# Kernel optimization log

Measured on AMD Instinct MI355X. Metric: run time of the kernel, lower is better.

## Reference

```python
import jax, jax.numpy as jnp
import numpy as np

B, C, Hf, Wf = 32, 512, 16, 16
S = Hf * Wf            # 256 kv tokens
D = 2048               # d_model
DIN = 512              # d_input (attention embed dim)
HEADS = 8
DH = DIN // HEADS
T = 50                 # iterations (internal ticks)
M = 25                 # memory_length
HH = 16                # memory_hidden_dims
NSA = 512              # n_synch_action
NSO = 512              # n_synch_out
OUT = 1000             # out_dims


def _ln(x, g, b, eps=1e-5):
    mu = x.mean(-1, keepdims=True)
    var = ((x - mu) ** 2).mean(-1, keepdims=True)
    return (x - mu) / jnp.sqrt(var + eps) * g + b


def _glu(x):
    a, b = jnp.split(x, 2, axis=-1)
    return a * jax.nn.sigmoid(b)


def setup_inputs() -> dict:
    key = jax.random.key(0)
    ki = iter(jax.random.split(key, 40))
    def rn(shape, s=0.02):
        return jax.random.normal(next(ki), shape, jnp.float32) * s
    inp = {}
    inp['x'] = jax.random.normal(next(ki), (B, C, Hf, Wf), jnp.float32)
    # kv_proj: Linear(C->DIN) + LayerNorm
    inp['kv_w'] = rn((C, DIN)); inp['kv_b'] = jnp.zeros((DIN,), jnp.float32)
    inp['ln_kv_g'] = jnp.ones((DIN,), jnp.float32); inp['ln_kv_b'] = jnp.zeros((DIN,), jnp.float32)
    # q_proj: Linear(NSA->DIN)
    inp['q_w'] = rn((NSA, DIN)); inp['q_b'] = jnp.zeros((DIN,), jnp.float32)
    # MultiheadAttention projections
    inp['Wq'] = rn((DIN, DIN)); inp['bq'] = jnp.zeros((DIN,), jnp.float32)
    inp['Wk'] = rn((DIN, DIN)); inp['bk'] = jnp.zeros((DIN,), jnp.float32)
    inp['Wv'] = rn((DIN, DIN)); inp['bv'] = jnp.zeros((DIN,), jnp.float32)
    inp['Wo'] = rn((DIN, DIN)); inp['bo'] = jnp.zeros((DIN,), jnp.float32)
    # synapse: Linear(DIN+D -> 2D) + GLU + LayerNorm(D)
    inp['syn_w'] = rn((DIN + D, 2 * D)); inp['syn_b'] = jnp.zeros((2 * D,), jnp.float32)
    inp['ln_syn_g'] = jnp.ones((D,), jnp.float32); inp['ln_syn_b'] = jnp.zeros((D,), jnp.float32)
    # per-neuron NLMs (SuperLinear weights: (in,out,N))
    inp['nlm_w1'] = rn((M, 2 * HH, D), 0.1); inp['nlm_b1'] = jnp.zeros((1, D, 2 * HH), jnp.float32)
    inp['nlm_w2'] = rn((HH, 2, D), 0.1); inp['nlm_b2'] = jnp.zeros((1, D, 2), jnp.float32)
    # output projector
    inp['out_w'] = rn((NSO, OUT)); inp['out_b'] = jnp.zeros((OUT,), jnp.float32)
    # learnable decay params (clamped to [0,15] in forward)
    inp['decay_action'] = jax.random.uniform(next(ki), (NSA,), jnp.float32)
    inp['decay_out'] = jax.random.uniform(next(ki), (NSO,), jnp.float32)
    # learned start state
    inp['start_trace'] = rn((D, M), 0.05)
    inp['start_act'] = rn((D,), 0.05)
    # random-pairing neuron indices (fixed at init in the original)
    inp['idx_la'] = jax.random.randint(next(ki), (NSA,), 0, D)
    inp['idx_ra'] = jax.random.randint(next(ki), (NSA,), 0, D)
    inp['idx_lo'] = jax.random.randint(next(ki), (NSO,), 0, D)
    inp['idx_ro'] = jax.random.randint(next(ki), (NSO,), 0, D)
    return inp


def reference(x, kv_w, kv_b, ln_kv_g, ln_kv_b, q_w, q_b, Wq, bq, Wk, bk, Wv, bv, Wo, bo,
              syn_w, syn_b, ln_syn_g, ln_syn_b, nlm_w1, nlm_b1, nlm_w2, nlm_b2,
              out_w, out_b, decay_action, decay_out, start_trace, start_act,
              idx_la, idx_ra, idx_lo, idx_ro):
    # featurise: identity backbone, flatten spatial to tokens, project to DIN
    feats = x.reshape(B, C, S).transpose(0, 2, 1)                 # (B,S,C)
    kv = _ln(feats @ kv_w + kv_b, ln_kv_g, ln_kv_b)               # (B,S,DIN)
    kh = (kv @ Wk + bk).reshape(B, S, HEADS, DH).transpose(0, 2, 1, 3)  # (B,H,S,DH)
    vh = (kv @ Wv + bv).reshape(B, S, HEADS, DH).transpose(0, 2, 1, 3)
    r_a = jnp.exp(-jnp.clip(decay_action, 0.0, 15.0))[None]       # (1,NSA)
    r_o = jnp.exp(-jnp.clip(decay_out, 0.0, 15.0))[None]          # (1,NSO)

    def nlm(trace):  # per-neuron MLP over the memory axis: (B,D,M) -> (B,D)
        h = _glu(jnp.einsum('bdm,mhd->bdh', trace, nlm_w1) + nlm_b1)
        return _glu(jnp.einsum('bdh,hod->bdo', h, nlm_w2) + nlm_b2)[..., 0]

    act0 = jnp.broadcast_to(start_act[None], (B, D))
    trace0 = jnp.broadcast_to(start_trace[None], (B, D, M))
    # out-synchronisation initialised from the start state (before the loop)
    a_o0 = act0[:, idx_lo] * act0[:, idx_ro]
    b_o0 = jnp.ones_like(a_o0)
    a_a0 = jnp.zeros((B, NSA), jnp.float32)
    b_a0 = jnp.zeros((B, NSA), jnp.float32)
    log_out = jnp.log(jnp.float32(OUT))
    scale = 1.0 / jnp.sqrt(jnp.float32(DH))

    def step(carry, _):
        trace, act, a_a, b_a, a_o, b_o = carry
        # action synchronisation (decayed pairwise products, sync = alpha/sqrt(beta))
        a_a = r_a * a_a + act[:, idx_la] * act[:, idx_ra]
        b_a = r_a * b_a + 1.0
        sync_a = a_a / jnp.sqrt(b_a)
        # attention readout (single query token)
        q = sync_a @ q_w + q_b                                    # (B,DIN)
        qh = (q @ Wq + bq).reshape(B, HEADS, 1, DH)
        attn = jax.nn.softmax(jnp.einsum('bhqd,bhkd->bhqk', qh, kh) * scale, -1)
        o = jnp.einsum('bhqk,bhkd->bhqd', attn, vh).transpose(0, 2, 1, 3).reshape(B, DIN)
        attn_out = o @ Wo + bo
        # synapse MLP -> new pre-activation state
        pre = jnp.concatenate([attn_out, act], axis=-1)           # (B,DIN+D)
        state = _ln(_glu(pre @ syn_w + syn_b), ln_syn_g, ln_syn_b)
        trace = jnp.concatenate([trace[:, :, 1:], state[:, :, None]], axis=-1)
        act = nlm(trace)                                          # (B,D)
        # output synchronisation + prediction
        a_o = r_o * a_o + act[:, idx_lo] * act[:, idx_ro]
        b_o = r_o * b_o + 1.0
        sync_o = a_o / jnp.sqrt(b_o)
        pred = sync_o @ out_w + out_b                             # (B,OUT)
        logp = jax.nn.log_softmax(pred, -1)
        ne = -(jnp.exp(logp) * logp).sum(-1) / log_out
        cert = jnp.stack([ne, 1.0 - ne], axis=-1)                 # (B,2)
        return (trace, act, a_a, b_a, a_o, b_o), (pred, cert, sync_o)

    _, (preds, certs, syncs) = jax.lax.scan(step, (trace0, act0, a_a0, b_a0, a_o0, b_o0), None, length=T)
    predictions = jnp.transpose(preds, (1, 2, 0))                 # (B,OUT,T)
    certainties = jnp.transpose(certs, (1, 2, 0))                 # (B,2,T)
    return predictions, certainties, syncs[-1]
```

## Files before the change

kernel.cpp:

```cpp
#include <hip/hip_runtime.h>
#include <math.h>

#define BB 32
#define CC 512
#define SS 256
#define DD 2048
#define DIN 512
#define NH 8
#define DHD 64
#define TT 50
#define MM 25
#define HHID 16
#define NSA 512
#define NSO 512
#define NOUT 1000

__device__ __forceinline__ unsigned short f2bf(float f) {
    unsigned u = __float_as_uint(f);
    u += 0x7fffu + ((u >> 16) & 1u);
    return (unsigned short)(u >> 16);
}
__device__ __forceinline__ float bf2f(unsigned short s) {
    return __uint_as_float((unsigned)s << 16);
}
__device__ __forceinline__ float blo(unsigned u) {
    return __uint_as_float(u << 16);
}
__device__ __forceinline__ float bhi(unsigned u) {
    return __uint_as_float(u & 0xffff0000u);
}

__global__ void init_kernel(const float* __restrict__ dec_a, const float* __restrict__ dec_o,
                            const float* __restrict__ start_act, const float* __restrict__ start_trace,
                            const int* __restrict__ idx_lo, const int* __restrict__ idx_ro,
                            float* __restrict__ r_a, float* __restrict__ r_o,
                            float* __restrict__ a_a, float* __restrict__ b_a,
                            float* __restrict__ a_o, float* __restrict__ b_o,
                            float* __restrict__ trace)
{
    int i = blockIdx.x * 256 + threadIdx.x;
    if (i < 512) {
        r_a[i] = expf(-fminf(fmaxf(dec_a[i], 0.f), 15.f));
        r_o[i] = expf(-fminf(fmaxf(dec_o[i], 0.f), 15.f));
    }
    if (i < BB * NSA) {
        a_a[i] = 0.f; b_a[i] = 0.f;
        int j = i & 511;
        a_o[i] = start_act[idx_lo[j]] * start_act[idx_ro[j]];
        b_o[i] = 1.f;
    }
    if (i < BB * MM * DD) {
        int rem = i % (MM * DD);
        int m = rem / DD, d = rem % DD;
        trace[i] = start_trace[d * MM + m];
    }
}

template<int AMODE, int SMODE>
__global__ void gemm64(const float* __restrict__ A, const float* __restrict__ Bm,
                       const float* __restrict__ bias, float* __restrict__ Cm,
                       int Mdim, int Ndim, int Kdim)
{
    __shared__ float As[16 * 65];
    __shared__ float Bs[16 * 64];
    int row0 = blockIdx.x * 64;
    int col0 = blockIdx.y * 64;
    int t = threadIdx.x;
    int tx = t & 15, ty = t >> 4;
    float acc[4][4] = {};
    for (int k0 = 0; k0 < Kdim; k0 += 16) {
        if (AMODE == 0) {
            for (int i = t; i < 1024; i += 256) {
                int kk = i & 15, r = i >> 4;
                As[kk * 65 + r] = A[(size_t)(row0 + r) * Kdim + k0 + kk];
            }
        } else {
            int b = row0 / SS, s0 = row0 % SS;
            for (int i = t; i < 1024; i += 256) {
                int r = i & 63, kk = i >> 6;
                As[kk * 65 + r] = A[((size_t)b * CC + k0 + kk) * SS + s0 + r];
            }
        }
        for (int i = t; i < 1024; i += 256) {
            int c = i & 63, kk = i >> 6;
            Bs[kk * 64 + c] = Bm[(size_t)(k0 + kk) * Ndim + col0 + c];
        }
        __syncthreads();
        #pragma unroll
        for (int kk = 0; kk < 16; ++kk) {
            float a[4], bb[4];
            #pragma unroll
            for (int i = 0; i < 4; i++) a[i] = As[kk * 65 + ty * 4 + i];
            #pragma unroll
            for (int j = 0; j < 4; j++) bb[j] = Bs[kk * 64 + tx * 4 + j];
            #pragma unroll
            for (int i = 0; i < 4; i++)
                #pragma unroll
                for (int j = 0; j < 4; j++) acc[i][j] += a[i] * bb[j];
        }
        __syncthreads();
    }
    #pragma unroll
    for (int i = 0; i < 4; i++)
        #pragma unroll
        for (int j = 0; j < 4; j++) {
            int row = row0 + ty * 4 + i, col = col0 + tx * 4 + j;
            float v = acc[i][j] + (bias ? bias[col] : 0.f);
            if (SMODE == 0) {
                Cm[(size_t)row * Ndim + col] = v;
            } else if (SMODE == 1) {
                int b = row / SS, s = row % SS, h = col >> 6, dh = col & 63;
                Cm[(((size_t)b * NH + h) * DHD + dh) * SS + s] = v;
            } else {
                int b = row / SS, s = row % SS, h = col >> 6, dh = col & 63;
                Cm[(((size_t)b * NH + h) * SS + s) * DHD + dh] = v;
            }
        }
}

__global__ void ln_rows(float* __restrict__ buf, const float* __restrict__ g,
                        const float* __restrict__ bta)
{
    int row = blockIdx.x, t = threadIdx.x;
    __shared__ float red[256];
    float v0 = buf[(size_t)row * 512 + t];
    float v1 = buf[(size_t)row * 512 + 256 + t];
    red[t] = v0 + v1; __syncthreads();
    for (int off = 128; off; off >>= 1) { if (t < off) red[t] += red[t + off]; __syncthreads(); }
    float mu = red[0] * (1.f / 512.f); __syncthreads();
    float d0 = v0 - mu, d1 = v1 - mu;
    red[t] = d0 * d0 + d1 * d1; __syncthreads();
    for (int off = 128; off; off >>= 1) { if (t < off) red[t] += red[t + off]; __syncthreads(); }
    float rstd = 1.f / sqrtf(red[0] * (1.f / 512.f) + 1e-5f);
    buf[(size_t)row * 512 + t]       = d0 * rstd * g[t] + bta[t];
    buf[(size_t)row * 512 + 256 + t] = d1 * rstd * g[t + 256] + bta[t + 256];
}

__global__ void bqq_kernel(const float* __restrict__ q_b, const float* __restrict__ Wq,
                           const float* __restrict__ bq, float* __restrict__ bqq)
{
    int c = blockIdx.x * 256 + threadIdx.x;
    if (c >= 512) return;
    float acc = bq[c];
    for (int k = 0; k < 512; k++) acc += q_b[k] * Wq[k * 512 + c];
    bqq[c] = acc;
}

__global__ void bias2_kernel(const float* __restrict__ bo, const float* __restrict__ syn_w,
                             const float* __restrict__ syn_b, float* __restrict__ bias2)
{
    int c = blockIdx.x * 256 + threadIdx.x;
    if (c >= 4096) return;
    float acc = syn_b[c];
    for (int k = 0; k < 512; k++) acc += bo[k] * syn_w[(size_t)k * 4096 + c];
    bias2[c] = acc;
}

__global__ void wt_build(const float* __restrict__ W2, const float* __restrict__ syn_w,
                         unsigned short* __restrict__ WTh)
{
    __shared__ float tile[32][33];
    int k0 = blockIdx.x * 32, c0 = blockIdx.y * 32;
    int t = threadIdx.x;
    int col = t & 31, rq = t >> 5;
    #pragma unroll
    for (int q = 0; q < 4; ++q) {
        int kk = q * 8 + rq;
        int k = k0 + kk;
        const float* src = (k < 512 ? W2 : syn_w) + (size_t)k * 4096 + c0;
        tile[kk][col] = src[col];
    }
    __syncthreads();
    #pragma unroll
    for (int q = 0; q < 4; ++q) {
        int cc = q * 8 + rq;
        WTh[(size_t)(c0 + cc) * 2560 + k0 + col] = f2bf(tile[col][cc]);
    }
}

__global__ void conv_kernel(const float* __restrict__ khT, const float* __restrict__ vh,
                            const float* __restrict__ w1,
                            unsigned short* __restrict__ khTh, unsigned short* __restrict__ vhh,
                            unsigned short* __restrict__ w1h)
{
    int i = blockIdx.x * 256 + threadIdx.x;
    khTh[i] = f2bf(khT[i]);
    vhh[i]  = f2bf(vh[i]);
    if (i < 25 * 32 * DD) w1h[i] = f2bf(w1[i]);
}

__global__ void act0_kernel(const float* __restrict__ start_act, float* __restrict__ act0slot)
{
    int i = blockIdx.x * 256 + threadIdx.x;
    if (i < BB * DD) act0slot[i] = start_act[i & (DD - 1)];
}

__global__ void pad_outw(const float* __restrict__ out_w, const float* __restrict__ out_b,
                         float* __restrict__ out_wp, float* __restrict__ out_bp)
{
    int i = blockIdx.x * 256 + threadIdx.x;
    if (i < 512 * 1024) {
        int r = i >> 10, c = i & 1023;
        out_wp[i] = (c < 1000) ? out_w[r * 1000 + c] : 0.f;
    }
    if (i < 1024) out_bp[i] = (i < 1000) ? out_b[i] : 0.f;
}

__global__ __launch_bounds__(256) void k1_front(
    const float* __restrict__ act, const int* __restrict__ la, const int* __restrict__ ra,
    const float* __restrict__ r_a,
    const float* __restrict__ aold, const float* __restrict__ bold,
    float* __restrict__ anew, float* __restrict__ bnew,
    const float* __restrict__ Wqq, const float* __restrict__ bqq,
    const unsigned short* __restrict__ khTh, const unsigned short* __restrict__ vhh,
    float* __restrict__ obuf)
{
    __shared__ float sa[512];
    __shared__ float qp[256];
    __shared__ float qs[64];
    __shared__ float ps[256];
    __shared__ float red[256];
    int bh = blockIdx.x, b = bh >> 3, h = bh & 7;
    int tid = threadIdx.x;
    const float* actb = act + b * DD;
    for (int j = tid; j < 512; j += 256) {
        float p = actb[la[j]] * actb[ra[j]];
        float r = r_a[j];
        float aa = r * aold[b * 512 + j] + p;
        float bb = r * bold[b * 512 + j] + 1.f;
        sa[j] = aa / sqrtf(bb);
        if (h == 0) { anew[b * 512 + j] = aa; bnew[b * 512 + j] = bb; }
    }
    __syncthreads();
    {
        int cl = tid & 63, q = tid >> 6;
        const float* wcol = Wqq + h * 64 + cl;
        float acc = 0.f;
        #pragma unroll 8
        for (int k = q * 128; k < q * 128 + 128; ++k)
            acc += sa[k] * wcol[k * 512];
        qp[tid] = acc;
    }
    __syncthreads();
    if (tid < 64)
        qs[tid] = qp[tid] + qp[tid + 64] + qp[tid + 128] + qp[tid + 192] + bqq[h * 64 + tid];
    __syncthreads();
    const unsigned short* kb = khTh + (size_t)bh * 64 * 256;
    float sc = 0.f;
    #pragma unroll 8
    for (int dh = 0; dh < 64; ++dh) sc += qs[dh] * bf2f(kb[dh * 256 + tid]);
    sc *= 0.125f;
    red[tid] = sc; __syncthreads();
    for (int off = 128; off; off >>= 1) { if (tid < off) red[tid] = fmaxf(red[tid], red[tid + off]); __syncthreads(); }
    float mx = red[0]; __syncthreads();
    float e = expf(sc - mx);
    red[tid] = e; __syncthreads();
    for (int off = 128; off; off >>= 1) { if (tid < off) red[tid] += red[tid + off]; __syncthreads(); }
    float inv = 1.f / red[0];
    ps[tid] = e * inv;
    __syncthreads();
    int dh = tid & 63, ch = tid >> 6;
    const unsigned short* vb = vhh + (size_t)bh * 256 * 64;
    float acc = 0.f;
    for (int s = ch * 64; s < ch * 64 + 64; ++s) acc += ps[s] * bf2f(vb[s * 64 + dh]);
    red[tid] = acc; __syncthreads();
    if (tid < 128) red[tid] += red[tid + 128];
    __syncthreads();
    if (tid < 64) obuf[b * 512 + h * 64 + tid] = red[tid] + red[tid + 64];
}

__global__ __launch_bounds__(256) void k2_glu(
    const float* __restrict__ obuf, const float* __restrict__ act,
    const unsigned short* __restrict__ WTh, const float* __restrict__ bias2,
    float* __restrict__ glbufT, float* __restrict__ partials)
{
    __shared__ float As[2 * 32 * 160];
    int tid = threadIdx.x, blk = blockIdx.x;
    int kh = tid >> 7;
    int cpair = (tid >> 5) & 3;
    int r = tid & 31;
    int c = blk * 4 + cpair;
    const unsigned short* wta = WTh + (size_t)c * 2560 + kh * 1280;
    const unsigned short* wtb = WTh + (size_t)(c + 2048) * 2560 + kh * 1280;
    float acc_a = 0.f, acc_b = 0.f;
    for (int ri = 0; ri < 8; ++ri) {
        __syncthreads();
        #pragma unroll
        for (int q = 0; q < 10; ++q) {
            int i = tid + q * 256;
            int hh = i / 1280;
            int rem = i - hh * 1280;
            int rr = rem / 40, kg = rem - (rem / 40) * 40;
            int k = hh * 1280 + ri * 160 + kg * 4;
            float4 v;
            if (k < 512) v = *(const float4*)(obuf + rr * 512 + k);
            else         v = *(const float4*)(act + rr * 2048 + (k - 512));
            *(float4*)(As + hh * 5120 + rr * 160 + ((kg ^ (rr & 7)) << 2)) = v;
        }
        __syncthreads();
        const float* Ar = As + kh * 5120 + r * 160;
        const unsigned short* wtaa = wta + ri * 160;
        const unsigned short* wtbb = wtb + ri * 160;
        int sw = r & 7;
        #pragma unroll 4
        for (int kc = 0; kc < 20; ++kc) {
            uint4 wa = *(const uint4*)(wtaa + kc * 8);
            uint4 wb = *(const uint4*)(wtbb + kc * 8);
            float4 a0 = *(const float4*)(Ar + (((2 * kc) ^ sw) << 2));
            float4 a1 = *(const float4*)(Ar + (((2 * kc + 1) ^ sw) << 2));
            acc_a += a0.x * blo(wa.x) + a0.y * bhi(wa.x) + a0.z * blo(wa.y) + a0.w * bhi(wa.y)
                   + a1.x * blo(wa.z) + a1.y * bhi(wa.z) + a1.z * blo(wa.w) + a1.w * bhi(wa.w);
            acc_b += a0.x * blo(wb.x) + a0.y * bhi(wb.x) + a0.z * blo(wb.y) + a0.w * bhi(wb.y)
                   + a1.x * blo(wb.z) + a1.y * bhi(wb.z) + a1.z * blo(wb.w) + a1.w * bhi(wb.w);
        }
    }
    __syncthreads();
    float* red_a = As;
    float* red_b = As + 128;
    float* gls   = As + 256;
    float* gl2s  = As + 384;
    if (kh == 1) {
        red_a[cpair * 32 + r] = acc_a;
        red_b[cpair * 32 + r] = acc_b;
    }
    __syncthreads();
    if (kh == 0) {
        float ua = acc_a + red_a[cpair * 32 + r] + bias2[c];
        float ub = acc_b + red_b[cpair * 32 + r] + bias2[c + 2048];
        float gl = ua * (1.f / (1.f + expf(-ub)));
        glbufT[c * 32 + r] = gl;
        gls[cpair * 32 + r] = gl;
        gl2s[cpair * 32 + r] = gl * gl;
    }
    __syncthreads();
    if (tid < 32) {
        float s = 0.f, s2 = 0.f;
        #pragma unroll
        for (int cp = 0; cp < 4; ++cp) { s += gls[cp * 32 + tid]; s2 += gl2s[cp * 32 + tid]; }
        partials[blk * 64 + tid * 2]     = s;
        partials[blk * 64 + tid * 2 + 1] = s2;
    }
}

#define K4_LDS_FLOATS (12800 + 2176 + 256 + 256 + 16)
__global__ __launch_bounds__(256) void k4_nlm(
    const float* __restrict__ glbufT, const float* __restrict__ partials,
    const float* __restrict__ g, const float* __restrict__ bta,
    float* __restrict__ trace,
    const unsigned short* __restrict__ w1h, const float* __restrict__ b1,
    const float* __restrict__ w2, const float* __restrict__ b2,
    float* __restrict__ actout, int t_iter)
{
    extern __shared__ float lds[];
    float* wlds  = lds;
    float* cross = lds + 12800;
    float* r1 = lds + 14976;
    float* r2 = lds + 15232;
    float* sm = lds + 15488;
    int tid = threadIdx.x, blk = blockIdx.x;
    int dtile = blk & 127, bgrp = blk >> 7;
    int d0 = dtile * 16, b0 = bgrp * 8;
    int hh = tid >> 7;
    int b_l = (tid >> 4) & 7;
    int d_l = tid & 15;
    int b = b0 + b_l, d = d0 + d_l;

    for (int q = 0; q < 50; ++q) {
        int i = tid + q * 256;
        wlds[i] = bf2f(w1h[(size_t)(i >> 4) * 2048 + d0 + (i & 15)]);
    }
    {
        int bb = tid >> 5, j = tid & 31;
        int bstat = b0 + bb;
        float s = 0.f, s2 = 0.f;
        #pragma unroll
        for (int q = 0; q < 16; ++q) {
            int kblk = j + 32 * q;
            s  += partials[kblk * 64 + bstat * 2];
            s2 += partials[kblk * 64 + bstat * 2 + 1];
        }
        r1[tid] = s; r2[tid] = s2;
        __syncthreads();
        for (int off = 16; off; off >>= 1) {
            if (j < off) { r1[tid] += r1[tid + off]; r2[tid] += r2[tid + off]; }
            __syncthreads();
        }
        if (j == 0) {
            float mu = r1[tid] * (1.f / 2048.f);
            float var = r2[tid] * (1.f / 2048.f) - mu * mu;
            sm[bb * 2] = mu;
            sm[bb * 2 + 1] = 1.f / sqrtf(var + 1e-5f);
        }
        __syncthreads();
    }
    float mu = sm[b_l * 2], rstd = sm[b_l * 2 + 1];
    float gl = glbufT[d * 32 + b];
    float nv = (gl - mu) * rstd * g[d] + bta[d];
    int newrow = t_iter % MM;
    if (hh == 0) trace[((size_t)b * MM + newrow) * DD + d] = nv;

    float hp[16];
    {
        const float* b1d = b1 + d * 32 + hh * 16;
        #pragma unroll
        for (int h = 0; h < 16; h++) hp[h] = b1d[h];
    }
    const float* trb = trace + (size_t)b * MM * DD + d;
    for (int m = 0; m < 24; m++) {
        int mph = (t_iter + 1 + m) % 25;
        float tv = trb[(size_t)mph * DD];
        const float* wm = wlds + (m * 32 + hh * 16) * 16 + d_l;
        #pragma unroll
        for (int h = 0; h < 16; h++) hp[h] += tv * wm[h * 16];
    }
    {
        const float* wm = wlds + (24 * 32 + hh * 16) * 16 + d_l;
        #pragma unroll
        for (int h = 0; h < 16; h++) hp[h] += nv * wm[h * 16];
    }
    if (hh == 1) {
        float* cx = cross + (b_l * 16 + d_l) * 17;
        #pragma unroll
        for (int h = 0; h < 16; h++) cx[h] = hp[h];
    }
    __syncthreads();
    if (hh == 0) {
        const float* cx = cross + (b_l * 16 + d_l) * 17;
        float o0 = b2[d * 2], o1 = b2[d * 2 + 1];
        #pragma unroll
        for (int h = 0; h < 16; h++) {
            float hv = hp[h] * (1.f / (1.f + expf(-cx[h])));
            o0 += hv * w2[((size_t)h * 2) * DD + d];
            o1 += hv * w2[((size_t)h * 2 + 1) * DD + d];
        }
        actout[b * DD + d] = o0 * (1.f / (1.f + expf(-o1)));
    }
}

__global__ __launch_bounds__(256) void k_syncscan(
    const float* __restrict__ acthist, const int* __restrict__ lo, const int* __restrict__ ro,
    const float* __restrict__ r_o,
    const float* __restrict__ a_o0, const float* __restrict__ b_o0,
    float* __restrict__ so_hist, float* __restrict__ out_sync)
{
    int idx = blockIdx.x * 256 + threadIdx.x;
    int b = idx >> 9, j = idx & 511;
    float aa = a_o0[idx], bb = b_o0[idx];
    float rr = r_o[j];
    int il = lo[j], ir = ro[j];
    const float* ah = acthist + (size_t)(BB * DD) + b * DD;
    float s = 0.f;
    for (int t = 0; t < TT; ++t) {
        float p = ah[il] * ah[ir];
        aa = rr * aa + p;
        bb = rr * bb + 1.f;
        s = aa / sqrtf(bb);
        so_hist[(size_t)t * (BB * 512) + idx] = s;
        ah += BB * DD;
    }
    out_sync[idx] = s;
}

__global__ __launch_bounds__(256) void k6_cert(
    const float* __restrict__ predt, float* __restrict__ d_out)
{
    int t_iter = blockIdx.x >> 5, b = blockIdx.x & 31, t = threadIdx.x;
    __shared__ float red[256];
    const float* pr = predt + ((size_t)t_iter * 32 + b) * 1024;
    float pv[4];
    float mx = -1e30f;
    #pragma unroll
    for (int ii = 0; ii < 4; ++ii) {
        int c = t + ii * 256;
        float v = -1e30f;
        if (c < 1000) {
            v = pr[c];
            d_out[(size_t)b * NOUT * TT + (size_t)c * TT + t_iter] = v;
        }
        pv[ii] = v;
        mx = fmaxf(mx, v);
    }
    red[t] = mx; __syncthreads();
    for (int off = 128; off; off >>= 1) { if (t < off) red[t] = fmaxf(red[t], red[t + off]); __syncthreads(); }
    mx = red[0]; __syncthreads();
    float s1 = 0.f, s2 = 0.f;
    #pragma unroll
    for (int ii = 0; ii < 4; ++ii) {
        int c = t + ii * 256;
        if (c < 1000) { float xx = pv[ii] - mx; float e = expf(xx); s1 += e; s2 += e * xx; }
    }
    red[t] = s1; __syncthreads();
    for (int off = 128; off; off >>= 1) { if (t < off) red[t] += red[t + off]; __syncthreads(); }
    s1 = red[0]; __syncthreads();
    red[t] = s2; __syncthreads();
    for (int off = 128; off; off >>= 1) { if (t < off) red[t] += red[t + off]; __syncthreads(); }
    s2 = red[0];
    if (t == 0) {
        float ne = -(s2 / s1 - logf(s1)) * (1.f / logf(1000.f));
        size_t base = (size_t)BB * NOUT * TT + (size_t)b * 2 * TT + t_iter;
        d_out[base] = ne;
        d_out[base + TT] = 1.f - ne;
    }
}

extern "C" void kernel_launch(void* const* d_in, const int* in_sizes, int n_in,
                              void* d_out, int out_size, void* d_ws, size_t ws_size,
                              hipStream_t stream)
{
    const float* x        = (const float*)d_in[0];
    const float* kv_w     = (const float*)d_in[1];
    const float* kv_b     = (const float*)d_in[2];
    const float* ln_kv_g  = (const float*)d_in[3];
    const float* ln_kv_b  = (const float*)d_in[4];
    const float* q_w      = (const float*)d_in[5];
    const float* q_b      = (const float*)d_in[6];
    const float* Wq       = (const float*)d_in[7];
    const float* bq       = (const float*)d_in[8];
    const float* Wk       = (const float*)d_in[9];
    const float* bk       = (const float*)d_in[10];
    const float* Wv       = (const float*)d_in[11];
    const float* bv       = (const float*)d_in[12];
    const float* Wo       = (const float*)d_in[13];
    const float* bo       = (const float*)d_in[14];
    const float* syn_w    = (const float*)d_in[15];
    const float* syn_b    = (const float*)d_in[16];
    const float* ln_syn_g = (const float*)d_in[17];
    const float* ln_syn_b = (const float*)d_in[18];
    const float* nlm_w1   = (const float*)d_in[19];
    const float* nlm_b1   = (const float*)d_in[20];
    const float* nlm_w2   = (const float*)d_in[21];
    const float* nlm_b2   = (const float*)d_in[22];
    const float* out_w    = (const float*)d_in[23];
    const float* out_b    = (const float*)d_in[24];
    const float* dec_a    = (const float*)d_in[25];
    const float* dec_o    = (const float*)d_in[26];
    const float* start_tr = (const float*)d_in[27];
    const float* start_ac = (const float*)d_in[28];
    const int*   idx_la   = (const int*)d_in[29];
    const int*   idx_ra   = (const int*)d_in[30];
    const int*   idx_lo   = (const int*)d_in[31];
    const int*   idx_ro   = (const int*)d_in[32];
    float* out = (float*)d_out;

    float* w = (float*)d_ws;
    float* kvbuf = w;            w += (size_t)8192 * 512;
    float* khT   = w;            w += (size_t)8192 * 512;
    float* vhb   = w;            w += (size_t)8192 * 512;
    float* Wqq   = w;            w += (size_t)512 * 512;
    float* bqq   = w;            w += 512;
    float* W2    = w;            w += (size_t)512 * 4096;
    float* bias2 = w;            w += 4096;
    float* r_a   = w;            w += 512;
    float* r_o   = w;            w += 512;
    float* a_a   = w;            w += 2 * BB * NSA;
    float* b_a   = w;            w += 2 * BB * NSA;
    float* a_o   = w;            w += BB * NSO;
    float* b_o   = w;            w += BB * NSO;
    float* trace = w;            w += (size_t)BB * MM * DD;
    float* obuf  = w;            w += BB * DIN;
    float* glbufT = w;           w += (size_t)DD * BB;
    float* partials = w;         w += 512 * 32 * 2;
    unsigned short* WTh  = (unsigned short*)w;  w += (size_t)4096 * 2560 / 2;
    unsigned short* khTh = (unsigned short*)w;  w += (size_t)8192 * 512 / 2;
    unsigned short* vhh  = (unsigned short*)w;  w += (size_t)8192 * 512 / 2;
    unsigned short* w1h  = (unsigned short*)w;  w += (size_t)25 * 32 * DD / 2;

    float* acthist = kvbuf;
    float* so_hist = vhb;
    float* predt   = vhb + 819200;
    float* out_wp  = khT;
    float* out_bp  = khT + 524288;

    init_kernel<<<6400, 256, 0, stream>>>(dec_a, dec_o, start_ac, start_tr, idx_lo, idx_ro,
                                          r_a, r_o, a_a, b_a, a_o, b_o, trace);
    gemm64<1, 0><<<dim3(128, 8), 256, 0, stream>>>(x, kv_w, kv_b, kvbuf, 8192, 512, 512);
    ln_rows<<<8192, 256, 0, stream>>>(kvbuf, ln_kv_g, ln_kv_b);
    gemm64<0, 1><<<dim3(128, 8), 256, 0, stream>>>(kvbuf, Wk, bk, khT, 8192, 512, 512);
    gemm64<0, 2><<<dim3(128, 8), 256, 0, stream>>>(kvbuf, Wv, bv, vhb, 8192, 512, 512);
    gemm64<0, 0><<<dim3(8, 8), 256, 0, stream>>>(q_w, Wq, nullptr, Wqq, 512, 512, 512);
    bqq_kernel<<<2, 256, 0, stream>>>(q_b, Wq, bq, bqq);
    gemm64<0, 0><<<dim3(8, 64), 256, 0, stream>>>(Wo, syn_w, nullptr, W2, 512, 4096, 512);
    bias2_kernel<<<16, 256, 0, stream>>>(bo, syn_w, syn_b, bias2);
    wt_build<<<dim3(80, 128), 256, 0, stream>>>(W2, syn_w, WTh);
    conv_kernel<<<16384, 256, 0, stream>>>(khT, vhb, nlm_w1, khTh, vhh, w1h);
    act0_kernel<<<256, 256, 0, stream>>>(start_ac, acthist);

    float* out_sync = out + (size_t)BB * NOUT * TT + (size_t)BB * 2 * TT;

    static int lds_attr_set = 0;
    if (!lds_attr_set) {
        hipFuncSetAttribute(reinterpret_cast<const void*>(k4_nlm),
                            hipFuncAttributeMaxDynamicSharedMemorySize,
                            K4_LDS_FLOATS * 4);
        lds_attr_set = 1;
    }

    for (int t = 0; t < TT; ++t) {
        int par = t & 1;
        const float* act_t = acthist + (size_t)t * (BB * DD);
        float* act_n = acthist + (size_t)(t + 1) * (BB * DD);
        k1_front<<<256, 256, 0, stream>>>(act_t, idx_la, idx_ra, r_a,
                                          a_a + par * (BB * 512), b_a + par * (BB * 512),
                                          a_a + (par ^ 1) * (BB * 512), b_a + (par ^ 1) * (BB * 512),
                                          Wqq, bqq, khTh, vhh, obuf);
        k2_glu<<<512, 256, 0, stream>>>(obuf, act_t, WTh, bias2, glbufT, partials);
        k4_nlm<<<512, 256, K4_LDS_FLOATS * 4, stream>>>(glbufT, partials,
                                            ln_syn_g, ln_syn_b, trace,
                                            w1h, nlm_b1, nlm_w2, nlm_b2, act_n, t);
    }

    k_syncscan<<<64, 256, 0, stream>>>(acthist, idx_lo, idx_ro, r_o, a_o, b_o,
                                       so_hist, out_sync);
    pad_outw<<<2048, 256, 0, stream>>>(out_w, out_b, out_wp, out_bp);
    gemm64<0, 0><<<dim3(25, 16), 256, 0, stream>>>(so_hist, out_wp, out_bp, predt,
                                                   1600, 1024, 512);
    k6_cert<<<1600, 256, 0, stream>>>(predt, out);
}
```

Before: 4.405 ms.

## Fuse per-tick attention, GLU and NLM kernels with grid-wide atomic barriers

Merges the three per-iteration kernels into one persistent-style launch of 512 blocks. The phases are separated by a software grid barrier built on an atomic counter. Intermediate buffers are indexed per tick so there is no reuse hazard across launches. The K/V projection GEMMs now write bf16 directly, which removes the separate conversion pass. This cuts launch count and launch gaps per tick, but the code depends on all 512 blocks being co-resident, and the spin barriers and cross-block visibility through relaxed atomics may add latency or risk deadlock.

Measured after the change: 5.317 ms. +20.7%, slower.

```diff
diff --git a/kernel.cpp b/kernel.cpp
--- a/kernel.cpp
+++ b/kernel.cpp
@@ -15,6 +15,9 @@
 #define NSO 512
 #define NOUT 1000
 
+#define NBLKT 512
+#define KT_LDS_FLOATS 15504
+
 __device__ __forceinline__ unsigned short f2bf(float f) {
     unsigned u = __float_as_uint(f);
     u += 0x7fffu + ((u >> 16) & 1u);
@@ -30,15 +33,34 @@
     return __uint_as_float(u & 0xffff0000u);
 }
 
+__device__ __forceinline__ void cst(float* p, float v) {
+    __hip_atomic_store(p, v, __ATOMIC_RELAXED, __HIP_MEMORY_SCOPE_AGENT);
+}
+
+__device__ __forceinline__ void gsync(unsigned* __restrict__ ctr, unsigned target)
+{
+    __threadfence_block();
+    __syncthreads();
+    if (threadIdx.x == 0) {
+        __hip_atomic_fetch_add(ctr, 1u, __ATOMIC_RELAXED, __HIP_MEMORY_SCOPE_AGENT);
+        while (__hip_atomic_load(ctr, __ATOMIC_RELAXED, __HIP_MEMORY_SCOPE_AGENT) < target)
+            __builtin_amdgcn_s_sleep(4);
+        asm volatile("" ::: "memory");
+    }
+    __syncthreads();
+}
+
 __global__ void init_kernel(const float* __restrict__ dec_a, const float* __restrict__ dec_o,
                             const float* __restrict__ start_act, const float* __restrict__ start_trace,
                             const int* __restrict__ idx_lo, const int* __restrict__ idx_ro,
+                            unsigned* __restrict__ bar,
                             float* __restrict__ r_a, float* __restrict__ r_o,
                             float* __restrict__ a_a, float* __restrict__ b_a,
                             float* __restrict__ a_o, float* __restrict__ b_o,
                             float* __restrict__ trace)
 {
     int i = blockIdx.x * 256 + threadIdx.x;
+    if (i < 16) bar[i] = 0u;
     if (i < 512) {
         r_a[i] = expf(-fminf(fmaxf(dec_a[i], 0.f), 15.f));
         r_o[i] = expf(-fminf(fmaxf(dec_o[i], 0.f), 15.f));
@@ -108,12 +130,12 @@
             float v = acc[i][j] + (bias ? bias[col] : 0.f);
             if (SMODE == 0) {
                 Cm[(size_t)row * Ndim + col] = v;
-            } else if (SMODE == 1) {
+            } else if (SMODE == 3) {
                 int b = row / SS, s = row % SS, h = col >> 6, dh = col & 63;
-                Cm[(((size_t)b * NH + h) * DHD + dh) * SS + s] = v;
-            } else {
+                ((unsigned short*)Cm)[(((size_t)b * NH + h) * DHD + dh) * SS + s] = f2bf(v);
+            } else if (SMODE == 4) {
                 int b = row / SS, s = row % SS, h = col >> 6, dh = col & 63;
-                Cm[(((size_t)b * NH + h) * SS + s) * DHD + dh] = v;
+                ((unsigned short*)Cm)[(((size_t)b * NH + h) * SS + s) * DHD + dh] = f2bf(v);
             }
         }
 }
@@ -178,14 +200,9 @@
     }
 }
 
-__global__ void conv_kernel(const float* __restrict__ khT, const float* __restrict__ vh,
-                            const float* __restrict__ w1,
-                            unsigned short* __restrict__ khTh, unsigned short* __restrict__ vhh,
-                            unsigned short* __restrict__ w1h)
+__global__ void conv_w1(const float* __restrict__ w1, unsigned short* __restrict__ w1h)
 {
     int i = blockIdx.x * 256 + threadIdx.x;
-    khTh[i] = f2bf(khT[i]);
-    vhh[i]  = f2bf(vh[i]);
     if (i < 25 * 32 * DD) w1h[i] = f2bf(w1[i]);
 }
 
@@ -206,234 +223,234 @@
     if (i < 1024) out_bp[i] = (i < 1000) ? out_b[i] : 0.f;
 }
 
-__global__ __launch_bounds__(256) void k1_front(
-    const float* __restrict__ act, const int* __restrict__ la, const int* __restrict__ ra,
+__global__ __launch_bounds__(256) void k_tick(
+    const float* __restrict__ act_t, float* __restrict__ act_n,
+    const int* __restrict__ la, const int* __restrict__ ra,
     const float* __restrict__ r_a,
     const float* __restrict__ aold, const float* __restrict__ bold,
     float* __restrict__ anew, float* __restrict__ bnew,
     const float* __restrict__ Wqq, const float* __restrict__ bqq,
     const unsigned short* __restrict__ khTh, const unsigned short* __restrict__ vhh,
-    float* __restrict__ obuf)
-{
-    __shared__ float sa[512];
-    __shared__ float qp[256];
-    __shared__ float qs[64];
-    __shared__ float ps[256];
-    __shared__ float red[256];
-    int bh = blockIdx.x, b = bh >> 3, h = bh & 7;
-    int tid = threadIdx.x;
-    const float* actb = act + b * DD;
-    for (int j = tid; j < 512; j += 256) {
-        float p = actb[la[j]] * actb[ra[j]];
-        float r = r_a[j];
-        float aa = r * aold[b * 512 + j] + p;
-        float bb = r * bold[b * 512 + j] + 1.f;
-        sa[j] = aa / sqrtf(bb);
-        if (h == 0) { anew[b * 512 + j] = aa; bnew[b * 512 + j] = bb; }
-    }
-    __syncthreads();
-    {
-        int cl = tid & 63, q = tid >> 6;
-        const float* wcol = Wqq + h * 64 + cl;
-        float acc = 0.f;
-        #pragma unroll 8
-        for (int k = q * 128; k < q * 128 + 128; ++k)
-            acc += sa[k] * wcol[k * 512];
-        qp[tid] = acc;
-    }
-    __syncthreads();
-    if (tid < 64)
-        qs[tid] = qp[tid] + qp[tid + 64] + qp[tid + 128] + qp[tid + 192] + bqq[h * 64 + tid];
-    __syncthreads();
-    const unsigned short* kb = khTh + (size_t)bh * 64 * 256;
-    float sc = 0.f;
-    #pragma unroll 8
-    for (int dh = 0; dh < 64; ++dh) sc += qs[dh] * bf2f(kb[dh * 256 + tid]);
-    sc *= 0.125f;
-    red[tid] = sc; __syncthreads();
-    for (int off = 128; off; off >>= 1) { if (tid < off) red[tid] = fmaxf(red[tid], red[tid + off]); __syncthreads(); }
-    float mx = red[0]; __syncthreads();
-    float e = expf(sc - mx);
-    red[tid] = e; __syncthreads();
-    for (int off = 128; off; off >>= 1) { if (tid < off) red[tid] += red[tid + off]; __syncthreads(); }
-    float inv = 1.f / red[0];
-    ps[tid] = e * inv;
-    __syncthreads();
-    int dh = tid & 63, ch = tid >> 6;
-    const unsigned short* vb = vhh + (size_t)bh * 256 * 64;
-    float acc = 0.f;
-    for (int s = ch * 64; s < ch * 64 + 64; ++s) acc += ps[s] * bf2f(vb[s * 64 + dh]);
-    red[tid] = acc; __syncthreads();
-    if (tid < 128) red[tid] += red[tid + 128];
-    __syncthreads();
-    if (tid < 64) obuf[b * 512 + h * 64 + tid] = red[tid] + red[tid + 64];
-}
-
-__global__ __launch_bounds__(256) void k2_glu(
-    const float* __restrict__ obuf, const float* __restrict__ act,
     const unsigned short* __restrict__ WTh, const float* __restrict__ bias2,
-    float* __restrict__ glbufT, float* __restrict__ partials)
-{
-    __shared__ float As[2 * 32 * 160];
-    int tid = threadIdx.x, blk = blockIdx.x;
-    int kh = tid >> 7;
-    int cpair = (tid >> 5) & 3;
-    int r = tid & 31;
-    int c = blk * 4 + cpair;
-    const unsigned short* wta = WTh + (size_t)c * 2560 + kh * 1280;
-    const unsigned short* wtb = WTh + (size_t)(c + 2048) * 2560 + kh * 1280;
-    float acc_a = 0.f, acc_b = 0.f;
-    for (int ri = 0; ri < 8; ++ri) {
-        __syncthreads();
-        #pragma unroll
-        for (int q = 0; q < 10; ++q) {
-            int i = tid + q * 256;
-            int hh = i / 1280;
-            int rem = i - hh * 1280;
-            int rr = rem / 40, kg = rem - (rem / 40) * 40;
-            int k = hh * 1280 + ri * 160 + kg * 4;
-            float4 v;
-            if (k < 512) v = *(const float4*)(obuf + rr * 512 + k);
-            else         v = *(const float4*)(act + rr * 2048 + (k - 512));
-            *(float4*)(As + hh * 5120 + rr * 160 + ((kg ^ (rr & 7)) << 2)) = v;
-        }
-        __syncthreads();
-        const float* Ar = As + kh * 5120 + r * 160;
-        const unsigned short* wtaa = wta + ri * 160;
-        const unsigned short* wtbb = wtb + ri * 160;
-        int sw = r & 7;
-        #pragma unroll 4
-        for (int kc = 0; kc < 20; ++kc) {
-            uint4 wa = *(const uint4*)(wtaa + kc * 8);
-            uint4 wb = *(const uint4*)(wtbb + kc * 8);
-            float4 a0 = *(const float4*)(Ar + (((2 * kc) ^ sw) << 2));
-            float4 a1 = *(const float4*)(Ar + (((2 * kc + 1) ^ sw) << 2));
-            acc_a += a0.x * blo(wa.x) + a0.y * bhi(wa.x) + a0.z * blo(wa.y) + a0.w * bhi(wa.y)
-                   + a1.x * blo(wa.z) + a1.y * bhi(wa.z) + a1.z * blo(wa.w) + a1.w * bhi(wa.w);
-            acc_b += a0.x * blo(wb.x) + a0.y * bhi(wb.x) + a0.z * blo(wb.y) + a0.w * bhi(wb.y)
-                   + a1.x * blo(wb.z) + a1.y * bhi(wb.z) + a1.z * blo(wb.w) + a1.w * bhi(wb.w);
-        }
-    }
-    __syncthreads();
-    float* red_a = As;
-    float* red_b = As + 128;
-    float* gls   = As + 256;
-    float* gl2s  = As + 384;
-    if (kh == 1) {
-        red_a[cpair * 32 + r] = acc_a;
-        red_b[cpair * 32 + r] = acc_b;
-    }
-    __syncthreads();
-    if (kh == 0) {
-        float ua = acc_a + red_a[cpair * 32 + r] + bias2[c];
-        float ub = acc_b + red_b[cpair * 32 + r] + bias2[c + 2048];
-        float gl = ua * (1.f / (1.f + expf(-ub)));
-        glbufT[c * 32 + r] = gl;
-        gls[cpair * 32 + r] = gl;
-        gl2s[cpair * 32 + r] = gl * gl;
-    }
-    __syncthreads();
-    if (tid < 32) {
-        float s = 0.f, s2 = 0.f;
-        #pragma unroll
-        for (int cp = 0; cp < 4; ++cp) { s += gls[cp * 32 + tid]; s2 += gl2s[cp * 32 + tid]; }
-        partials[blk * 64 + tid * 2]     = s;
-        partials[blk * 64 + tid * 2 + 1] = s2;
-    }
-}
-
-#define K4_LDS_FLOATS (12800 + 2176 + 256 + 256 + 16)
-__global__ __launch_bounds__(256) void k4_nlm(
-    const float* __restrict__ glbufT, const float* __restrict__ partials,
     const float* __restrict__ g, const float* __restrict__ bta,
     float* __restrict__ trace,
     const unsigned short* __restrict__ w1h, const float* __restrict__ b1,
     const float* __restrict__ w2, const float* __restrict__ b2,
-    float* __restrict__ actout, int t_iter)
+    float* __restrict__ obuf_t, float* __restrict__ gl_t, float* __restrict__ part_t,
+    unsigned* __restrict__ bar, int t_iter)
 {
     extern __shared__ float lds[];
-    float* wlds  = lds;
-    float* cross = lds + 12800;
-    float* r1 = lds + 14976;
-    float* r2 = lds + 15232;
-    float* sm = lds + 15488;
-    int tid = threadIdx.x, blk = blockIdx.x;
-    int dtile = blk & 127, bgrp = blk >> 7;
-    int d0 = dtile * 16, b0 = bgrp * 8;
-    int hh = tid >> 7;
-    int b_l = (tid >> 4) & 7;
-    int d_l = tid & 15;
-    int b = b0 + b_l, d = d0 + d_l;
-
-    for (int q = 0; q < 50; ++q) {
-        int i = tid + q * 256;
-        wlds[i] = bf2f(w1h[(size_t)(i >> 4) * 2048 + d0 + (i & 15)]);
-    }
+    const int blk = blockIdx.x;
+    const int tid = threadIdx.x;
+    const unsigned base = (unsigned)t_iter * (2u * NBLKT);
+
+    if (blk < 256) {
+        float* sa  = lds;
+        float* qp  = lds + 512;
+        float* qs  = lds + 768;
+        float* ps  = lds + 832;
+        float* red = lds + 1088;
+        int b = blk >> 3, h = blk & 7;
+        const float* actb = act_t + b * DD;
+        for (int j = tid; j < 512; j += 256) {
+            float p = actb[la[j]] * actb[ra[j]];
+            float r = r_a[j];
+            float aa = r * aold[b * 512 + j] + p;
+            float bb = r * bold[b * 512 + j] + 1.f;
+            sa[j] = aa / sqrtf(bb);
+            if (h == 0) { anew[b * 512 + j] = aa; bnew[b * 512 + j] = bb; }
+        }
+        __syncthreads();
+        {
+            int cl = tid & 63, q = tid >> 6;
+            const float* wcol = Wqq + h * 64 + cl;
+            float acc = 0.f;
+            #pragma unroll 8
+            for (int k = q * 128; k < q * 128 + 128; ++k)
+                acc += sa[k] * wcol[k * 512];
+            qp[tid] = acc;
+        }
+        __syncthreads();
+        if (tid < 64)
+            qs[tid] = qp[tid] + qp[tid + 64] + qp[tid + 128] + qp[tid + 192] + bqq[h * 64 + tid];
+        __syncthreads();
+        const unsigned short* kb = khTh + (size_t)blk * 64 * 256;
+        float sc = 0.f;
+        #pragma unroll 8
+        for (int dh = 0; dh < 64; ++dh) sc += qs[dh] * bf2f(kb[dh * 256 + tid]);
+        sc *= 0.125f;
+        red[tid] = sc; __syncthreads();
+        for (int off = 128; off; off >>= 1) { if (tid < off) red[tid] = fmaxf(red[tid], red[tid + off]); __syncthreads(); }
+        float mx = red[0]; __syncthreads();
+        float e = expf(sc - mx);
+        red[tid] = e; __syncthreads();
+        for (int off = 128; off; off >>= 1) { if (tid < off) red[tid] += red[tid + off]; __syncthreads(); }
+        float inv = 1.f / red[0];
+        ps[tid] = e * inv;
+        __syncthreads();
+        int dh = tid & 63, ch = tid >> 6;
+        const unsigned short* vb = vhh + (size_t)blk * 256 * 64;
+        float acc = 0.f;
+        for (int s = ch * 64; s < ch * 64 + 64; ++s) acc += ps[s] * bf2f(vb[s * 64 + dh]);
+        red[tid] = acc; __syncthreads();
+        if (tid < 128) red[tid] += red[tid + 128];
+        __syncthreads();
+        if (tid < 64) cst(&obuf_t[b * 512 + h * 64 + tid], red[tid] + red[tid + 64]);
+    }
+    gsync(bar, base + NBLKT);
+
     {
-        int bb = tid >> 5, j = tid & 31;
-        int bstat = b0 + bb;
-        float s = 0.f, s2 = 0.f;
-        #pragma unroll
-        for (int q = 0; q < 16; ++q) {
-            int kblk = j + 32 * q;
-            s  += partials[kblk * 64 + bstat * 2];
-            s2 += partials[kblk * 64 + bstat * 2 + 1];
-        }
-        r1[tid] = s; r2[tid] = s2;
-        __syncthreads();
-        for (int off = 16; off; off >>= 1) {
-            if (j < off) { r1[tid] += r1[tid + off]; r2[tid] += r2[tid + off]; }
+        float* As = lds;
+        int kh = tid >> 7;
+        int cpair = (tid >> 5) & 3;
+        int r = tid & 31;
+        int c = blk * 4 + cpair;
+        const unsigned short* wta = WTh + (size_t)c * 2560 + kh * 1280;
+        const unsigned short* wtb = WTh + (size_t)(c + 2048) * 2560 + kh * 1280;
+        float acc_a = 0.f, acc_b = 0.f;
+        for (int ri = 0; ri < 8; ++ri) {
             __syncthreads();
-        }
-        if (j == 0) {
-            float mu = r1[tid] * (1.f / 2048.f);
-            float var = r2[tid] * (1.f / 2048.f) - mu * mu;
-            sm[bb * 2] = mu;
-            sm[bb * 2 + 1] = 1.f / sqrtf(var + 1e-5f);
-        }
-        __syncthreads();
-    }
-    float mu = sm[b_l * 2], rstd = sm[b_l * 2 + 1];
-    float gl = glbufT[d * 32 + b];
-    float nv = (gl - mu) * rstd * g[d] + bta[d];
-    int newrow = t_iter % MM;
-    if (hh == 0) trace[((size_t)b * MM + newrow) * DD + d] = nv;
-
-    float hp[16];
+            #pragma unroll
+            for (int q = 0; q < 10; ++q) {
+                int i = tid + q * 256;
+                int hh = i / 1280;
+                int rem = i - hh * 1280;
+                int rr = rem / 40, kg = rem - (rem / 40) * 40;
+                int k = hh * 1280 + ri * 160 + kg * 4;
+                float4 v;
+                if (k < 512) v = *(const float4*)(obuf_t + rr * 512 + k);
+                else         v = *(const float4*)(act_t + rr * 2048 + (k - 512));
+                *(float4*)(As + hh * 5120 + rr * 160 + ((kg ^ (rr & 7)) << 2)) = v;
+            }
+            __syncthreads();
+            const float* Ar = As + kh * 5120 + r * 160;
+            const unsigned short* wtaa = wta + ri * 160;
+            const unsigned short* wtbb = wtb + ri * 160;
+            int sw = r & 7;
+            #pragma unroll 4
+            for (int kc = 0; kc < 20; ++kc) {
+                uint4 wa = *(const uint4*)(wtaa + kc * 8);
+                uint4 wb = *(const uint4*)(wtbb + kc * 8);
+                float4 a0 = *(const float4*)(Ar + (((2 * kc) ^ sw) << 2));
+                float4 a1 = *(const float4*)(Ar + (((2 * kc + 1) ^ sw) << 2));
+                acc_a += a0.x * blo(wa.x) + a0.y * bhi(wa.x) + a0.z * blo(wa.y) + a0.w * bhi(wa.y)
+                       + a1.x * blo(wa.z) + a1.y * bhi(wa.z) + a1.z * blo(wa.w) + a1.w * bhi(wa.w);
+                acc_b += a0.x * blo(wb.x) + a0.y * bhi(wb.x) + a0.z * blo(wb.y) + a0.w * bhi(wb.y)
+                       + a1.x * blo(wb.z) + a1.y * bhi(wb.z) + a1.z * blo(wb.w) + a1.w * bhi(wb.w);
+            }
+        }
+        __syncthreads();
+        float* red_a = lds;
+        float* red_b = lds + 128;
+        float* gls   = lds + 256;
+        float* gl2s  = lds + 384;
+        if (kh == 1) {
+            red_a[cpair * 32 + r] = acc_a;
+            red_b[cpair * 32 + r] = acc_b;
+        }
+        __syncthreads();
+        if (kh == 0) {
+            float ua = acc_a + red_a[cpair * 32 + r] + bias2[c];
+            float ub = acc_b + red_b[cpair * 32 + r] + bias2[c + 2048];
+            float gl = ua * (1.f / (1.f + expf(-ub)));
+            cst(&gl_t[c * 32 + r], gl);
+            gls[cpair * 32 + r] = gl;
+            gl2s[cpair * 32 + r] = gl * gl;
+        }
+        __syncthreads();
+        if (tid < 32) {
+            float s = 0.f, s2 = 0.f;
+            #pragma unroll
+            for (int cp = 0; cp < 4; ++cp) { s += gls[cp * 32 + tid]; s2 += gl2s[cp * 32 + tid]; }
+            cst(&part_t[blk * 64 + tid * 2], s);
+            cst(&part_t[blk * 64 + tid * 2 + 1], s2);
+        }
+    }
+    gsync(bar, base + 2 * NBLKT);
+
     {
-        const float* b1d = b1 + d * 32 + hh * 16;
-        #pragma unroll
-        for (int h = 0; h < 16; h++) hp[h] = b1d[h];
-    }
-    const float* trb = trace + (size_t)b * MM * DD + d;
-    for (int m = 0; m < 24; m++) {
-        int mph = (t_iter + 1 + m) % 25;
-        float tv = trb[(size_t)mph * DD];
-        const float* wm = wlds + (m * 32 + hh * 16) * 16 + d_l;
-        #pragma unroll
-        for (int h = 0; h < 16; h++) hp[h] += tv * wm[h * 16];
-    }
-    {
-        const float* wm = wlds + (24 * 32 + hh * 16) * 16 + d_l;
-        #pragma unroll
-        for (int h = 0; h < 16; h++) hp[h] += nv * wm[h * 16];
-    }
-    if (hh == 1) {
-        float* cx = cross + (b_l * 16 + d_l) * 17;
-        #pragma unroll
-        for (int h = 0; h < 16; h++) cx[h] = hp[h];
-    }
-    __syncthreads();
-    if (hh == 0) {
-        const float* cx = cross + (b_l * 16 + d_l) * 17;
-        float o0 = b2[d * 2], o1 = b2[d * 2 + 1];
-        #pragma unroll
-        for (int h = 0; h < 16; h++) {
-            float hv = hp[h] * (1.f / (1.f + expf(-cx[h])));
-            o0 += hv * w2[((size_t)h * 2) * DD + d];
-            o1 += hv * w2[((size_t)h * 2 + 1) * DD + d];
-        }
-        actout[b * DD + d] = o0 * (1.f / (1.f + expf(-o1)));
+        float* wlds  = lds;
+        float* cross = lds + 12800;
+        float* r1 = lds + 14976;
+        float* r2 = lds + 15232;
+        float* sm = lds + 15488;
+        int dtile = blk & 127, bgrp = blk >> 7;
+        int d0 = dtile * 16, b0 = bgrp * 8;
+        int hh = tid >> 7;
+        int b_l = (tid >> 4) & 7;
+        int d_l = tid & 15;
+        int b = b0 + b_l, d = d0 + d_l;
+
+        for (int q = 0; q < 50; ++q) {
+            int i = tid + q * 256;
+            wlds[i] = bf2f(w1h[(size_t)(i >> 4) * 2048 + d0 + (i & 15)]);
+        }
+        {
+            int bb = tid >> 5, j = tid & 31;
+            int bstat = b0 + bb;
+            float s = 0.f, s2 = 0.f;
+            #pragma unroll
+            for (int q = 0; q < 16; ++q) {
+                int kblk = j + 32 * q;
+                s  += part_t[kblk * 64 + bstat * 2];
+                s2 += part_t[kblk * 64 + bstat * 2 + 1];
+            }
+            r1[tid] = s; r2[tid] = s2;
+            __syncthreads();
+            for (int off = 16; off; off >>= 1) {
+                if (j < off) { r1[tid] += r1[tid + off]; r2[tid] += r2[tid + off]; }
+                __syncthreads();
+            }
+            if (j == 0) {
+                float mu = r1[tid] * (1.f / 2048.f);
+                float var = r2[tid] * (1.f / 2048.f) - mu * mu;
+                sm[bb * 2] = mu;
+                sm[bb * 2 + 1] = 1.f / sqrtf(var + 1e-5f);
+            }
+            __syncthreads();
+        }
+        float mu = sm[b_l * 2], rstd = sm[b_l * 2 + 1];
+        float gl = gl_t[d * 32 + b];
+        float nv = (gl - mu) * rstd * g[d] + bta[d];
+        int newrow = t_iter % MM;
+        if (hh == 0) trace[((size_t)b * MM + newrow) * DD + d] = nv;
+
+        float hp[16];
+        {
+            const float* b1d = b1 + d * 32 + hh * 16;
+            #pragma unroll
+            for (int h = 0; h < 16; h++) hp[h] = b1d[h];
+        }
+        const float* trb = trace + (size_t)b * MM * DD + d;
+        for (int m = 0; m < 24; m++) {
+            int mph = (t_iter + 1 + m) % 25;
+            float tv = trb[(size_t)mph * DD];
+            const float* wm = wlds + (m * 32 + hh * 16) * 16 + d_l;
+            #pragma unroll
+            for (int h = 0; h < 16; h++) hp[h] += tv * wm[h * 16];
+        }
+        {
+            const float* wm = wlds + (24 * 32 + hh * 16) * 16 + d_l;
+            #pragma unroll
+            for (int h = 0; h < 16; h++) hp[h] += nv * wm[h * 16];
+        }
+        if (hh == 1) {
+            float* cx = cross + (b_l * 16 + d_l) * 17;
+            #pragma unroll
+            for (int h = 0; h < 16; h++) cx[h] = hp[h];
+        }
+        __syncthreads();
+        if (hh == 0) {
+            const float* cx = cross + (b_l * 16 + d_l) * 17;
+            float o0 = b2[d * 2], o1 = b2[d * 2 + 1];
+            #pragma unroll
+            for (int h = 0; h < 16; h++) {
+                float hv = hp[h] * (1.f / (1.f + expf(-cx[h])));
+                o0 += hv * w2[((size_t)h * 2) * DD + d];
+                o1 += hv * w2[((size_t)h * 2 + 1) * DD + d];
+            }
+            act_n[b * DD + d] = o0 * (1.f / (1.f + expf(-o1)));
+        }
     }
 }
 
@@ -542,10 +559,11 @@
     const int*   idx_ro   = (const int*)d_in[32];
     float* out = (float*)d_out;
 
-    float* w = (float*)d_ws;
+    unsigned* bar = (unsigned*)d_ws;
+    float* w = (float*)d_ws + 64;
     float* kvbuf = w;            w += (size_t)8192 * 512;
-    float* khT   = w;            w += (size_t)8192 * 512;
-    float* vhb   = w;            w += (size_t)8192 * 512;
+    float* bigA  = w;            w += (size_t)8192 * 512;
+    float* bigB  = w;            w += (size_t)8192 * 512;
     float* Wqq   = w;            w += (size_t)512 * 512;
     float* bqq   = w;            w += 512;
     float* W2    = w;            w += (size_t)512 * 4096;
@@ -557,41 +575,41 @@
     float* a_o   = w;            w += BB * NSO;
     float* b_o   = w;            w += BB * NSO;
     float* trace = w;            w += (size_t)BB * MM * DD;
-    float* obuf  = w;            w += BB * DIN;
-    float* glbufT = w;           w += (size_t)DD * BB;
-    float* partials = w;         w += 512 * 32 * 2;
     unsigned short* WTh  = (unsigned short*)w;  w += (size_t)4096 * 2560 / 2;
     unsigned short* khTh = (unsigned short*)w;  w += (size_t)8192 * 512 / 2;
     unsigned short* vhh  = (unsigned short*)w;  w += (size_t)8192 * 512 / 2;
     unsigned short* w1h  = (unsigned short*)w;  w += (size_t)25 * 32 * DD / 2;
 
     float* acthist = kvbuf;
-    float* so_hist = vhb;
-    float* predt   = vhb + 819200;
-    float* out_wp  = khT;
-    float* out_bp  = khT + 524288;
+    float* glR     = bigA;
+    float* out_wp  = bigA + 3276800;
+    float* out_bp  = out_wp + 524288;
+    float* obufR   = bigB;
+    float* partR   = bigB + 819200;
+    float* so_hist = bigB;
+    float* predt   = bigB + 819200;
 
     init_kernel<<<6400, 256, 0, stream>>>(dec_a, dec_o, start_ac, start_tr, idx_lo, idx_ro,
-                                          r_a, r_o, a_a, b_a, a_o, b_o, trace);
+                                          bar, r_a, r_o, a_a, b_a, a_o, b_o, trace);
     gemm64<1, 0><<<dim3(128, 8), 256, 0, stream>>>(x, kv_w, kv_b, kvbuf, 8192, 512, 512);
     ln_rows<<<8192, 256, 0, stream>>>(kvbuf, ln_kv_g, ln_kv_b);
-    gemm64<0, 1><<<dim3(128, 8), 256, 0, stream>>>(kvbuf, Wk, bk, khT, 8192, 512, 512);
-    gemm64<0, 2><<<dim3(128, 8), 256, 0, stream>>>(kvbuf, Wv, bv, vhb, 8192, 512, 512);
+    gemm64<0, 3><<<dim3(128, 8), 256, 0, stream>>>(kvbuf, Wk, bk, (float*)khTh, 8192, 512, 512);
+    gemm64<0, 4><<<dim3(128, 8), 256, 0, stream>>>(kvbuf, Wv, bv, (float*)vhh, 8192, 512, 512);
     gemm64<0, 0><<<dim3(8, 8), 256, 0, stream>>>(q_w, Wq, nullptr, Wqq, 512, 512, 512);
     bqq_kernel<<<2, 256, 0, stream>>>(q_b, Wq, bq, bqq);
     gemm64<0, 0><<<dim3(8, 64), 256, 0, stream>>>(Wo, syn_w, nullptr, W2, 512, 4096, 512);
     bias2_kernel<<<16, 256, 0, stream>>>(bo, syn_w, syn_b, bias2);
     wt_build<<<dim3(80, 128), 256, 0, stream>>>(W2, syn_w, WTh);
-    conv_kernel<<<16384, 256, 0, stream>>>(khT, vhb, nlm_w1, khTh, vhh, w1h);
+    conv_w1<<<6400, 256, 0, stream>>>(nlm_w1, w1h);
     act0_kernel<<<256, 256, 0, stream>>>(start_ac, acthist);
 
     float* out_sync = out + (size_t)BB * NOUT * TT + (size_t)BB * 2 * TT;
 
     static int lds_attr_set = 0;
     if (!lds_attr_set) {
-        hipFuncSetAttribute(reinterpret_cast<const void*>(k4_nlm),
+        hipFuncSetAttribute(reinterpret_cast<const void*>(k_tick),
                             hipFuncAttributeMaxDynamicSharedMemorySize,
-                            K4_LDS_FLOATS * 4);
+                            KT_LDS_FLOATS * 4);
         lds_attr_set = 1;
     }
 
@@ -599,14 +617,17 @@
         int par = t & 1;
         const float* act_t = acthist + (size_t)t * (BB * DD);
         float* act_n = acthist + (size_t)(t + 1) * (BB * DD);
-        k1_front<<<256, 256, 0, stream>>>(act_t, idx_la, idx_ra, r_a,
-                                          a_a + par * (BB * 512), b_a + par * (BB * 512),
-                                          a_a + (par ^ 1) * (BB * 512), b_a + (par ^ 1) * (BB * 512),
-                                          Wqq, bqq, khTh, vhh, obuf);
-        k2_glu<<<512, 256, 0, stream>>>(obuf, act_t, WTh, bias2, glbufT, partials);
-        k4_nlm<<<512, 256, K4_LDS_FLOATS * 4, stream>>>(glbufT, partials,
-                                            ln_syn_g, ln_syn_b, trace,
-                                            w1h, nlm_b1, nlm_w2, nlm_b2, act_n, t);
+        k_tick<<<NBLKT, 256, KT_LDS_FLOATS * 4, stream>>>(
+            act_t, act_n, idx_la, idx_ra, r_a,
+            a_a + par * (BB * 512), b_a + par * (BB * 512),
+            a_a + (par ^ 1) * (BB * 512), b_a + (par ^ 1) * (BB * 512),
+            Wqq, bqq, khTh, vhh, WTh, bias2,
+            ln_syn_g, ln_syn_b, trace,
+            w1h, nlm_b1, nlm_w2, nlm_b2,
+            obufR + (size_t)t * (BB * DIN),
+            glR + (size_t)t * (DD * BB),
+            partR + (size_t)t * (NBLKT * 64),
+            bar, t);
     }
 
     k_syncscan<<<64, 256, 0, stream>>>(acthist, idx_lo, idx_ro, r_o, a_o, b_o,
```
